# Optimization experiments

Measured on AMD Instinct MI355X. Metric: run time of the kernel, lower is better.

The kernel has to match this reference:

```python
import jax, jax.numpy as jnp
import numpy as np

B, T = 64, 512
OBS, DM, DS, NL = 115, 128, 8, 3
EMB, NA, H1 = 16, 19, 256


def _ln(x, g, b, eps=1e-5):
    m = jnp.mean(x, -1, keepdims=True)
    v = jnp.mean((x - m) ** 2, -1, keepdims=True)
    return (x - m) * jax.lax.rsqrt(v + eps) * g + b


def _s6(x, h, lng, lnb, w_ig, w_dt, b_dt, a_log, w_b, w_c, d_par, w_out):
    # x: [B,T,DM], h: [B,DM,DS]
    xn = _ln(x, lng, lnb)
    xp = xn @ w_ig.T                               # [B,T,2*DM]
    x_in, z = xp[..., :DM], xp[..., DM:]
    dt = jax.nn.softplus(x_in @ w_dt.T + b_dt)     # [B,T,DM]
    A = -jnp.exp(a_log)                            # [DM,DS]
    bt = x_in @ w_b.T                              # [B,T,DS]
    ct = x_in @ w_c.T                              # [B,T,DS]
    dA = jnp.exp(dt[..., None] * A)                # [B,T,DM,DS]
    upd = (dt * x_in)[..., None] * bt[:, :, None, :]  # [B,T,DM,DS]

    def step(hc, inp):
        dA_t, u_t, c_t = inp
        hn = dA_t * hc + u_t                       # [B,DM,DS]
        y = jnp.einsum('bds,bs->bd', hn, c_t)      # [B,DM]
        return hn, y

    h_f, ys = jax.lax.scan(
        step, h,
        (jnp.swapaxes(dA, 0, 1), jnp.swapaxes(upd, 0, 1), jnp.swapaxes(ct, 0, 1)))
    y = jnp.swapaxes(ys, 0, 1)                     # [B,T,DM]
    ssm = y * jax.nn.silu(z) + x_in * d_par
    return x + ssm @ w_out.T, h_f.reshape(h_f.shape[0], -1)


def _forward(prev_actions, obs, h0, enc_w1, enc_b1, enc_g1, enc_bb1, enc_w2, enc_b2,
             enc_g2, enc_bb2, emb, proj_w, proj_b, proj_g, proj_bb,
             m_ln_g, m_ln_b, m_w_ig, m_w_dt, m_b_dt, m_a_log, m_w_b, m_w_c, m_d, m_w_out,
             fn_g, fn_b, pol_w1, pol_b1, pol_g, pol_bb, pol_w2, pol_b2):
    # MLP encoder: Linear -> LN -> SiLU -> Linear -> LN (final norm)
    e = jax.nn.silu(_ln(obs @ enc_w1.T + enc_b1, enc_g1, enc_bb1))
    e = _ln(e @ enc_w2.T + enc_b2, enc_g2, enc_bb2)
    pa = emb[prev_actions]                         # [B,T,EMB]
    x = jnp.concatenate([e, pa], -1) @ proj_w.T + proj_b
    x = jax.nn.silu(_ln(x, proj_g, proj_bb))
    for i in range(NL):
        x, _ = _s6(x, h0[i].reshape(-1, DM, DS), m_ln_g[i], m_ln_b[i], m_w_ig[i],
                   m_w_dt[i], m_b_dt[i], m_a_log[i], m_w_b[i], m_w_c[i], m_d[i], m_w_out[i])
    x = _ln(x, fn_g, fn_b)
    p = jax.nn.silu(_ln(x @ pol_w1.T + pol_b1, pol_g, pol_bb))
    return p @ pol_w2.T + pol_b2                   # [B,T,NA] policy logits


def setup_inputs() -> dict:
    key = jax.random.key(0)
    ks = iter(jax.random.split(key, 64))
    def n(shape, s=0.05):
        return jax.random.normal(next(ks), shape, dtype=jnp.float32) * s
    return {
        'obs': jax.random.normal(next(ks), (B, T, OBS), dtype=jnp.float32),
        'h0': jnp.zeros((NL, B, DM * DS), jnp.float32),
        'enc_w1': n((H1, OBS)), 'enc_b1': jnp.zeros((H1,)),
        'enc_g1': jnp.ones((H1,)), 'enc_bb1': jnp.zeros((H1,)),
        'enc_w2': n((DM, H1)), 'enc_b2': jnp.zeros((DM,)),
        'enc_g2': jnp.ones((DM,)), 'enc_bb2': jnp.zeros((DM,)),
        'emb': n((NA + 1, EMB), 1.0),
        'proj_w': n((DM, DM + EMB)), 'proj_b': jnp.zeros((DM,)),
        'proj_g': jnp.ones((DM,)), 'proj_bb': jnp.zeros((DM,)),
        'm_ln_g': jnp.ones((NL, DM)), 'm_ln_b': jnp.zeros((NL, DM)),
        'm_w_ig': n((NL, 2 * DM, DM)), 'm_w_dt': n((NL, DM, DM)),
        'm_b_dt': jnp.zeros((NL, DM)),
        'm_a_log': jax.random.uniform(next(ks), (NL, DM, DS), minval=-3.0, maxval=-1.0, dtype=jnp.float32),
        'm_w_b': n((NL, DS, DM)), 'm_w_c': n((NL, DS, DM)),
        'm_d': jnp.ones((NL, DM)), 'm_w_out': n((NL, DM, DM)),
        'fn_g': jnp.ones((DM,)), 'fn_b': jnp.zeros((DM,)),
        'pol_w1': n((DM, DM)), 'pol_b1': jnp.zeros((DM,)),
        'pol_g': jnp.ones((DM,)), 'pol_bb': jnp.zeros((DM,)),
        'pol_w2': n((NA, DM)), 'pol_b2': jnp.zeros((NA,)),
        'prev_actions': jax.random.randint(next(ks), (B, T), 0, NA + 1),
    }


def reference(obs, h0, enc_w1, enc_b1, enc_g1, enc_bb1, enc_w2, enc_b2, enc_g2, enc_bb2,
              emb, proj_w, proj_b, proj_g, proj_bb, m_ln_g, m_ln_b, m_w_ig, m_w_dt,
              m_b_dt, m_a_log, m_w_b, m_w_c, m_d, m_w_out, fn_g, fn_b, pol_w1, pol_b1,
              pol_g, pol_bb, pol_w2, pol_b2, prev_actions):
    return _forward(prev_actions, obs, h0, enc_w1, enc_b1, enc_g1, enc_bb1, enc_w2,
                    enc_b2, enc_g2, enc_bb2, emb, proj_w, proj_b, proj_g, proj_bb,
                    m_ln_g, m_ln_b, m_w_ig, m_w_dt, m_b_dt, m_a_log, m_w_b, m_w_c,
                    m_d, m_w_out, fn_g, fn_b, pol_w1, pol_b1, pol_g, pol_bb, pol_w2, pol_b2)
```

## Files before the change

### kernel.cpp

```cpp
#include <hip/hip_runtime.h>
#include <math.h>

#define BB 64
#define TT 512
#define OBSD 115
#define DMD 128
#define DSD 8
#define NLD 3
#define EMBD 16
#define NAD 19
#define H1D 256
#define NTOK (BB*TT)
#define SSEG 16
#define TSEG (TT/SSEG)

typedef unsigned short ushort_t;
typedef __attribute__((ext_vector_type(8))) short short8;
typedef __attribute__((ext_vector_type(4))) float f32x4;

__device__ __forceinline__ float silu_f(float x){ return x / (1.f + __expf(-x)); }
__device__ __forceinline__ float softplus_f(float x){
  return fmaxf(x, 0.f) + log1pf(__expf(-fabsf(x)));
}
__device__ __forceinline__ ushort_t f2bf(float x){
  unsigned u = __float_as_uint(x);
  unsigned r = (u + 0x7fffu + ((u >> 16) & 1u)) >> 16;
  return (ushort_t)r;
}
__device__ __forceinline__ float b2f(ushort_t x){
  return __uint_as_float(((unsigned)x) << 16);
}
#define MFMA(a,b,c) __builtin_amdgcn_mfma_f32_16x16x32_bf16((a),(b),(c),0,0,0)
#define LOG2E 1.44269504f

template<int D, int SV>
__device__ __forceinline__ void ln32(const float* s_val, float* s_mr, int tid){
  const int t = tid >> 3, part = tid & 7;
  float s = 0.f, s2 = 0.f;
  #pragma unroll
  for (int j = part; j < D; j += 8){ float v = s_val[t*SV + j]; s += v; s2 = fmaf(v, v, s2); }
  s += __shfl_xor(s, 1, 64); s2 += __shfl_xor(s2, 1, 64);
  s += __shfl_xor(s, 2, 64); s2 += __shfl_xor(s2, 2, 64);
  s += __shfl_xor(s, 4, 64); s2 += __shfl_xor(s2, 4, 64);
  if (part == 0){
    float m = s * (1.f/(float)D);
    s_mr[t*2] = m;
    s_mr[t*2+1] = rsqrtf(s2 * (1.f/(float)D) - m*m + 1e-5f);
  }
}

struct PJob { const float* src; ushort_t* dst; int N; int K; int Kpad; int rowofs; int Nw; };
struct PJobs { PJob j[20]; };

__global__ __launch_bounds__(256) void k_prep(PJobs P){
  const int job = blockIdx.x >> 2;
  const int sub = blockIdx.x & 3;
  PJob pj = P.j[job];
  const int elems = pj.Nw * pj.Kpad;
  for (int idx = sub*256 + threadIdx.x; idx < elems; idx += 4*256){
    int n = idx / pj.Kpad;
    int k = idx - n*pj.Kpad;
    float v = (n < pj.N && k < pj.K) ? pj.src[(size_t)n*pj.K + k] : 0.f;
    pj.dst[(size_t)(pj.rowofs + n)*pj.Kpad + k] = f2bf(v);
  }
}

__global__ __launch_bounds__(256) void k_enc1(
    const float* __restrict__ obs, const ushort_t* __restrict__ w1b,
    const float* __restrict__ b1, const float* __restrict__ g1,
    const float* __restrict__ bb1, ushort_t* __restrict__ e1)
{
  __shared__ __align__(16) char sm[34048];
  float*    s_val = (float*)sm;
  ushort_t* s_a   = (ushort_t*)sm;
  float*    s_mr  = (float*)(sm + 33792);
  const int tok0 = blockIdx.x * 32;
  const int tid = threadIdx.x;
  const int lane = tid & 63, w = tid >> 6;
  const int q = lane >> 4, cn = lane & 15;
  const int m0 = (w & 1) * 16, nh = w >> 1;

  for (int e = tid; e < 32*16; e += 256){
    int t = e >> 4, kc = e & 15;
    const float* op = obs + (size_t)(tok0 + t)*OBSD;
    short8 v;
    #pragma unroll
    for (int j = 0; j < 8; j++){
      int k = kc*8 + j;
      v[j] = (short)f2bf(k < OBSD ? op[k] : 0.f);
    }
    *(short8*)&s_a[t*136 + kc*8] = v;
  }
  __syncthreads();

  short8 af[4];
  #pragma unroll
  for (int ks = 0; ks < 4; ks++)
    af[ks] = *(const short8*)&s_a[(m0 + cn)*136 + ks*32 + q*8];
  __syncthreads();

  #pragma unroll
  for (int nt = 0; nt < 8; nt++){
    const int n0 = (nh*8 + nt) * 16;
    f32x4 acc = {0.f,0.f,0.f,0.f};
    #pragma unroll
    for (int ks = 0; ks < 4; ks++){
      short8 bf = *(const short8*)&w1b[(size_t)(n0 + cn)*128 + ks*32 + q*8];
      acc = MFMA(af[ks], bf, acc);
    }
    float bias = b1[n0 + cn];
    #pragma unroll
    for (int r = 0; r < 4; r++)
      s_val[(m0 + q*4 + r)*264 + n0 + cn] = acc[r] + bias;
  }
  __syncthreads();

  ln32<256,264>(s_val, s_mr, tid);
  __syncthreads();
  for (int e = tid; e < 32*256; e += 256){
    int t = e >> 8, c = e & 255;
    float v = (s_val[t*264 + c] - s_mr[t*2]) * s_mr[t*2+1] * g1[c] + bb1[c];
    e1[(size_t)(tok0 + t)*256 + c] = f2bf(silu_f(v));
  }
}

__global__ __launch_bounds__(256) void k_enc2p(
    const ushort_t* __restrict__ e1, const ushort_t* __restrict__ w2b,
    const float* __restrict__ b2, const float* __restrict__ g2,
    const float* __restrict__ bb2,
    const float* __restrict__ emb, const int* __restrict__ pact,
    const ushort_t* __restrict__ pwb, const float* __restrict__ pb,
    const float* __restrict__ pg, const float* __restrict__ pbb,
    float* __restrict__ X,
    const float* __restrict__ lng, const float* __restrict__ lnb,
    const ushort_t* __restrict__ wigb, const ushort_t* __restrict__ wdbcb,
    const float* __restrict__ bdt,
    ushort_t* __restrict__ XINb, ushort_t* __restrict__ Zb,
    ushort_t* __restrict__ DTb, ushort_t* __restrict__ BTu, ushort_t* __restrict__ CTu,
    const float* __restrict__ alog0,
    float* __restrict__ HLOC, float* __restrict__ PPR)
{
  __shared__ __align__(16) char sm[28928];
  float*    s_val = (float*)sm;
  ushort_t* s_xin = (ushort_t*)sm;
  ushort_t* s_dt  = (ushort_t*)(sm + 8704);
  ushort_t* s_a   = (ushort_t*)(sm + 17408);
  ushort_t* s_btc = (ushort_t*)(sm + 28160);
  float*    s_mr  = (float*)(sm + 28672);

  const int tok0 = blockIdx.x * 32;
  const int bidx = blockIdx.x >> 4;
  const int ch   = blockIdx.x & 15;
  const int tid = threadIdx.x;
  const int lane = tid & 63, w = tid >> 6;
  const int q = lane >> 4, cn = lane & 15;
  const int m0 = (w & 1) * 16, nh = w >> 1;

  for (int e = tid; e < 32*32; e += 256){
    int t = e >> 5, k = e & 31;
    float v = 0.f;
    if (k < EMBD){ int a = pact[tok0 + t]; v = emb[(size_t)a*EMBD + k]; }
    s_a[t*168 + 128 + k] = f2bf(v);
  }
  {
    short8 af[8];
    #pragma unroll
    for (int ks = 0; ks < 8; ks++)
      af[ks] = *(const short8*)&e1[(size_t)(tok0 + m0 + cn)*256 + ks*32 + q*8];
    #pragma unroll
    for (int nt = 0; nt < 4; nt++){
      const int n0 = (nh*4 + nt) * 16;
      f32x4 acc = {0.f,0.f,0.f,0.f};
      #pragma unroll
      for (int ks = 0; ks < 8; ks++){
        short8 bf = *(const short8*)&w2b[(size_t)(n0 + cn)*256 + ks*32 + q*8];
        acc = MFMA(af[ks], bf, acc);
      }
      float bias = b2[n0 + cn];
      #pragma unroll
      for (int r = 0; r < 4; r++)
        s_val[(m0 + q*4 + r)*136 + n0 + cn] = acc[r] + bias;
    }
  }
  __syncthreads();

  ln32<128,136>(s_val, s_mr, tid);
  __syncthreads();
  for (int e = tid; e < 32*128; e += 256){
    int t = e >> 7, c = e & 127;
    float v = (s_val[t*136 + c] - s_mr[t*2]) * s_mr[t*2+1] * g2[c] + bb2[c];
    s_a[t*168 + c] = f2bf(v);
  }
  __syncthreads();

  {
    short8 af2[5];
    #pragma unroll
    for (int ks = 0; ks < 5; ks++)
      af2[ks] = *(const short8*)&s_a[(m0 + cn)*168 + ks*32 + q*8];
    #pragma unroll
    for (int nt = 0; nt < 4; nt++){
      const int n0 = (nh*4 + nt) * 16;
      f32x4 acc = {0.f,0.f,0.f,0.f};
      #pragma unroll
      for (int ks = 0; ks < 5; ks++){
        short8 bf = *(const short8*)&pwb[(size_t)(n0 + cn)*160 + ks*32 + q*8];
        acc = MFMA(af2[ks], bf, acc);
      }
      float bias = pb[n0 + cn];
      #pragma unroll
      for (int r = 0; r < 4; r++)
        s_val[(m0 + q*4 + r)*136 + n0 + cn] = acc[r] + bias;
    }
  }
  __syncthreads();

  ln32<128,136>(s_val, s_mr, tid);
  __syncthreads();
  for (int e = tid; e < 32*128; e += 256){
    int t = e >> 7, c = e & 127;
    float v = (s_val[t*136 + c] - s_mr[t*2]) * s_mr[t*2+1] * pg[c] + pbb[c];
    v = silu_f(v);
    X[(size_t)tok0*128 + e] = v;
    s_val[t*136 + c] = v;
  }
  __syncthreads();

  ln32<128,136>(s_val, s_mr, tid);
  __syncthreads();
  for (int e = tid; e < 32*128; e += 256){
    int t = e >> 7, c = e & 127;
    float v = (s_val[t*136 + c] - s_mr[t*2]) * s_mr[t*2+1] * lng[c] + lnb[c];
    s_a[t*168 + c] = f2bf(v);
  }
  __syncthreads();

  {
    short8 af[4];
    #pragma unroll
    for (int ks = 0; ks < 4; ks++)
      af[ks] = *(const short8*)&s_a[(m0 + cn)*168 + ks*32 + q*8];
    #pragma unroll
    for (int nt = 0; nt < 8; nt++){
      const int n0 = (nh*8 + nt) * 16;
      f32x4 acc = {0.f,0.f,0.f,0.f};
      #pragma unroll
      for (int ks = 0; ks < 4; ks++){
        short8 bf = *(const short8*)&wigb[(size_t)(n0 + cn)*128 + ks*32 + q*8];
        acc = MFMA(af[ks], bf, acc);
      }
      if (n0 < 128){
        #pragma unroll
        for (int r = 0; r < 4; r++){
          int tr = m0 + q*4 + r;
          ushort_t bb = f2bf(acc[r]);
          XINb[(size_t)(tok0 + tr)*128 + n0 + cn] = bb;
          s_xin[tr*136 + n0 + cn] = bb;
        }
      } else {
        #pragma unroll
        for (int r = 0; r < 4; r++){
          int tr = m0 + q*4 + r;
          Zb[(size_t)(tok0 + tr)*128 + (n0 - 128) + cn] = f2bf(acc[r]);
        }
      }
    }
  }
  __syncthreads();

  {
    short8 af2[4];
    #pragma unroll
    for (int ks = 0; ks < 4; ks++)
      af2[ks] = *(const short8*)&s_xin[(m0 + cn)*136 + ks*32 + q*8];
    for (int nt = nh; nt < 9; nt += 2){
      const int n0 = nt * 16;
      f32x4 acc = {0.f,0.f,0.f,0.f};
      #pragma unroll
      for (int ks = 0; ks < 4; ks++){
        short8 bf = *(const short8*)&wdbcb[(size_t)(n0 + cn)*128 + ks*32 + q*8];
        acc = MFMA(af2[ks], bf, acc);
      }
      const int col = n0 + cn;
      if (col < 128){
        float bd = bdt[col];
        #pragma unroll
        for (int r = 0; r < 4; r++){
          int tr = m0 + q*4 + r;
          ushort_t dv = f2bf(softplus_f(acc[r] + bd));
          DTb[(size_t)(tok0 + tr)*128 + col] = dv;
          s_dt[tr*136 + col] = dv;
        }
      } else if (col < 136){
        #pragma unroll
        for (int r = 0; r < 4; r++){
          int tr = m0 + q*4 + r;
          ushort_t bb = f2bf(acc[r]);
          BTu[(size_t)(tok0 + tr)*8 + (col - 128)] = bb;
          s_btc[tr*8 + (col - 128)] = bb;
        }
      } else {
        #pragma unroll
        for (int r = 0; r < 4; r++)
          CTu[(size_t)(tok0 + m0 + q*4 + r)*8 + (col - 136)] = f2bf(acc[r]);
      }
    }
  }
  __syncthreads();

  {
    const int d = tid & 127, sh = tid >> 7;
    float A2c[4], hh[4], pp[4];
    #pragma unroll
    for (int j = 0; j < 4; j++){
      A2c[j] = -__expf(alog0[d*8 + sh*4 + j]) * LOG2E;
      hh[j] = 0.f; pp[j] = 1.f;
    }
    for (int t = 0; t < 32; t++){
      float dt = b2f(s_dt[t*136 + d]);
      float wv = dt * b2f(s_xin[t*136 + d]);
      #pragma unroll
      for (int j = 0; j < 4; j++){
        float dA = exp2f(dt * A2c[j]);
        hh[j] = fmaf(dA, hh[j], wv * b2f(s_btc[t*8 + sh*4 + j]));
        pp[j] *= dA;
      }
    }
    const size_t o = ((size_t)bidx*16 + ch)*1024 + d*8 + sh*4;
    #pragma unroll
    for (int j = 0; j < 4; j++){ HLOC[o+j] = hh[j]; PPR[o+j] = pp[j]; }
  }
}

#define SMS 26368

__device__ __forceinline__ void phaseB_post(
    const ushort_t* DTb, const ushort_t* XINb, const ushort_t* Zb,
    const ushort_t* BTu, const ushort_t* CTu,
    const float* __restrict__ alog, const float* __restrict__ h0g,
    const float* __restrict__ HLi, const float* __restrict__ PPi,
    const float* __restrict__ dpar, const ushort_t* __restrict__ woutb,
    float* __restrict__ X, char* sm, int b, int sg, int tid)
{
  ushort_t* s_dtS = (ushort_t*)sm;
  ushort_t* s_xiS = (ushort_t*)(sm + 8192);
  ushort_t* s_a   = (ushort_t*)(sm + 16384);
  float*    s_x   = (float*)sm;
  ushort_t* s_bt  = (ushort_t*)(sm + 25088);
  ushort_t* s_ct  = (ushort_t*)(sm + 25600);
  float*    s_mr  = (float*)(sm + 26112);

  const int d = tid;
  const int w = tid >> 6, lane = tid & 63, q = lane >> 4, cn = lane & 15;
  const size_t segtok = (size_t)b*TT + sg*TSEG;

  {
    const uint4* gdt = (const uint4*)(DTb + segtok*128);
    const uint4* gxi = (const uint4*)(XINb + segtok*128);
    #pragma unroll
    for (int i = 0; i < 4; i++){
      ((uint4*)s_dtS)[tid + i*128] = gdt[tid + i*128];
      ((uint4*)s_xiS)[tid + i*128] = gxi[tid + i*128];
    }
    ((unsigned*)s_bt)[tid] = ((const unsigned*)(BTu + segtok*8))[tid];
    ((unsigned*)s_ct)[tid] = ((const unsigned*)(CTu + segtok*8))[tid];
  }
  float A2[8], h[8];
  #pragma unroll
  for (int s = 0; s < 8; s++){
    A2[s] = -__expf(alog[d*8 + s]) * LOG2E;
    h[s] = h0g[(size_t)b*1024 + d*8 + s];
  }
  for (int ch = 0; ch < sg; ch++){
    const size_t o = ((size_t)b*SSEG + ch)*1024 + d*8;
    float4 hl0 = *(const float4*)(HLi + o);
    float4 hl1 = *(const float4*)(HLi + o + 4);
    float4 pp0 = *(const float4*)(PPi + o);
    float4 pp1 = *(const float4*)(PPi + o + 4);
    h[0]=fmaf(pp0.x,h[0],hl0.x); h[1]=fmaf(pp0.y,h[1],hl0.y);
    h[2]=fmaf(pp0.z,h[2],hl0.z); h[3]=fmaf(pp0.w,h[3],hl0.w);
    h[4]=fmaf(pp1.x,h[4],hl1.x); h[5]=fmaf(pp1.y,h[5],hl1.y);
    h[6]=fmaf(pp1.z,h[6],hl1.z); h[7]=fmaf(pp1.w,h[7],hl1.w);
  }
  __syncthreads();

  #pragma unroll 4
  for (int t = 0; t < 32; t++){
    float dt = b2f(s_dtS[t*128 + d]);
    float xi = b2f(s_xiS[t*128 + d]);
    float wv = dt * xi;
    float y = 0.f;
    #pragma unroll
    for (int s = 0; s < 8; s++){
      float dA = exp2f(dt * A2[s]);
      h[s] = fmaf(dA, h[s], wv * b2f(s_bt[t*8 + s]));
      y = fmaf(h[s], b2f(s_ct[t*8 + s]), y);
    }
    s_a[t*136 + d] = f2bf(y);
  }
  __syncthreads();

  {
    const int c0 = (tid & 15)*8, trow = tid >> 4;
    float dpv[8];
    #pragma unroll
    for (int j = 0; j < 8; j++) dpv[j] = dpar[c0 + j];
    #pragma unroll
    for (int i = 0; i < 4; i++){
      const int t = trow + i*8;
      uint4 zb = ((const uint4*)(Zb + segtok*128))[tid + i*128];
      const ushort_t* zp = (const ushort_t*)&zb;
      #pragma unroll
      for (int j = 0; j < 8; j++){
        float y  = b2f(s_a[t*136 + c0 + j]);
        float xi = b2f(s_xiS[t*128 + c0 + j]);
        float ssm = y * silu_f(b2f(zp[j])) + xi * dpv[j];
        s_a[t*136 + c0 + j] = f2bf(ssm);
      }
    }
  }
  __syncthreads();

  {
    short8 af[2][4];
    #pragma unroll
    for (int mt = 0; mt < 2; mt++)
      #pragma unroll
      for (int ks = 0; ks < 4; ks++)
        af[mt][ks] = *(const short8*)&s_a[(mt*16 + cn)*136 + ks*32 + q*8];
    __syncthreads();
    for (int nt = w; nt < 8; nt += 2){
      const int n0 = nt * 16;
      short8 bf[4];
      #pragma unroll
      for (int ks = 0; ks < 4; ks++)
        bf[ks] = *(const short8*)&woutb[(size_t)(n0+cn)*128 + ks*32 + q*8];
      #pragma unroll
      for (int mt = 0; mt < 2; mt++){
        f32x4 acc = {0.f,0.f,0.f,0.f};
        #pragma unroll
        for (int ks = 0; ks < 4; ks++) acc = MFMA(af[mt][ks], bf[ks], acc);
        #pragma unroll
        for (int r = 0; r < 4; r++){
          const int tr = mt*16 + q*4 + r;
          const size_t g = (segtok + tr)*128 + n0 + cn;
          float xn = X[g] + acc[r];
          X[g] = xn;
          s_x[tr*130 + n0 + cn] = xn;
        }
      }
    }
  }
  __syncthreads();

  {
    const int t = tid >> 2, qtr = tid & 3;
    float s = 0.f, s2 = 0.f;
    const float* row = s_x + t*130 + qtr*32;
    for (int j = 0; j < 32; j++){ float v = row[j]; s += v; s2 = fmaf(v, v, s2); }
    s  += __shfl_xor(s, 1, 64);  s2 += __shfl_xor(s2, 1, 64);
    s  += __shfl_xor(s, 2, 64);  s2 += __shfl_xor(s2, 2, 64);
    float m = s * (1.f/128.f);
    float var = s2 * (1.f/128.f) - m*m;
    if (qtr == 0){ s_mr[t*2] = m; s_mr[t*2+1] = rsqrtf(var + 1e-5f); }
  }
  __syncthreads();
}

__global__ __launch_bounds__(256) void k_scan2p(
    ushort_t* DTb, ushort_t* XINb, ushort_t* Zb,
    ushort_t* BTu, ushort_t* CTu,
    const float* __restrict__ alog, const float* __restrict__ h0g,
    const float* __restrict__ HLi, const float* __restrict__ PPi,
    const float* __restrict__ dpar, const ushort_t* __restrict__ woutb,
    float* __restrict__ X,
    const float* __restrict__ lng, const float* __restrict__ lnb,
    const ushort_t* __restrict__ wigb, const ushort_t* __restrict__ wdbcb,
    const float* __restrict__ bdt,
    const float* __restrict__ alogn,
    float* __restrict__ HLo, float* __restrict__ PPo)
{
  __shared__ __align__(16) char sm_all[2*SMS];
  const int sub = threadIdx.x >> 7;
  char* sm = sm_all + sub*SMS;
  const int tid = threadIdx.x & 127;

  ushort_t* s_a  = (ushort_t*)(sm + 16384);
  float*    s_x  = (float*)sm;
  ushort_t* s_xin= (ushort_t*)sm;
  ushort_t* s_bt = (ushort_t*)(sm + 25088);
  float*    s_mr = (float*)(sm + 26112);

  const int b = blockIdx.x >> 3;
  const int sg = (blockIdx.x & 7)*2 + sub;
  const int w = tid >> 6, lane = tid & 63, q = lane >> 4, cn = lane & 15;
  const size_t segtok = (size_t)b*TT + sg*TSEG;

  phaseB_post(DTb, XINb, Zb, BTu, CTu, alog, h0g, HLi, PPi, dpar, woutb, X, sm, b, sg, tid);

  {
    float g = lng[tid], c0 = lnb[tid];
    float x31 = s_x[31*130 + tid];
    __syncthreads();
    for (int t = 0; t < 31; t++){
      float v = (s_x[t*130 + tid] - s_mr[t*2]) * s_mr[t*2+1] * g + c0;
      s_a[t*136 + tid] = f2bf(v);
    }
    float v = (x31 - s_mr[62]) * s_mr[63] * g + c0;
    s_a[31*136 + tid] = f2bf(v);
  }
  __syncthreads();

  {
    short8 af[2][4];
    #pragma unroll
    for (int mt = 0; mt < 2; mt++)
      #pragma unroll
      for (int ks = 0; ks < 4; ks++)
        af[mt][ks] = *(const short8*)&s_a[(mt*16 + cn)*136 + ks*32 + q*8];
    for (int nt = w; nt < 16; nt += 2){
      const int n0 = nt * 16;
      short8 bf[4];
      #pragma unroll
      for (int ks = 0; ks < 4; ks++)
        bf[ks] = *(const short8*)&wigb[(size_t)(n0+cn)*128 + ks*32 + q*8];
      #pragma unroll
      for (int mt = 0; mt < 2; mt++){
        f32x4 acc = {0.f,0.f,0.f,0.f};
        #pragma unroll
        for (int ks = 0; ks < 4; ks++) acc = MFMA(af[mt][ks], bf[ks], acc);
        if (n0 < 128){
          #pragma unroll
          for (int r = 0; r < 4; r++){
            const int tr = mt*16 + q*4 + r;
            ushort_t bb = f2bf(acc[r]);
            XINb[(segtok + tr)*128 + n0 + cn] = bb;
            s_xin[tr*136 + n0 + cn] = bb;
          }
        } else {
          #pragma unroll
          for (int r = 0; r < 4; r++){
            const int tr = mt*16 + q*4 + r;
            Zb[(segtok + tr)*128 + (n0-128) + cn] = f2bf(acc[r]);
          }
        }
      }
    }
  }
  __syncthreads();

  {
    short8 af[2][4];
    #pragma unroll
    for (int mt = 0; mt < 2; mt++)
      #pragma unroll
      for (int ks = 0; ks < 4; ks++)
        af[mt][ks] = *(const short8*)&s_xin[(mt*16 + cn)*136 + ks*32 + q*8];
    for (int nt = w; nt < 9; nt += 2){
      const int n0 = nt * 16;
      short8 bf[4];
      #pragma unroll
      for (int ks = 0; ks < 4; ks++)
        bf[ks] = *(const short8*)&wdbcb[(size_t)(n0+cn)*128 + ks*32 + q*8];
      const int col = n0 + cn;
      #pragma unroll
      for (int mt = 0; mt < 2; mt++){
        f32x4 acc = {0.f,0.f,0.f,0.f};
        #pragma unroll
        for (int ks = 0; ks < 4; ks++) acc = MFMA(af[mt][ks], bf[ks], acc);
        if (col < 128){
          float bd = bdt[col];
          #pragma unroll
          for (int r = 0; r < 4; r++){
            const int tr = mt*16 + q*4 + r;
            ushort_t dv = f2bf(softplus_f(acc[r] + bd));
            DTb[(segtok + tr)*128 + col] = dv;
            s_a[tr*136 + col] = dv;
          }
        } else if (col < 136){
          #pragma unroll
          for (int r = 0; r < 4; r++){
            const int tr = mt*16 + q*4 + r;
            ushort_t bb = f2bf(acc[r]);
            BTu[(segtok + tr)*8 + (col-128)] = bb;
            s_bt[tr*8 + (col-128)] = bb;
          }
        } else {
          #pragma unroll
          for (int r = 0; r < 4; r++)
            CTu[(segtok + mt*16 + q*4 + r)*8 + (col-136)] = f2bf(acc[r]);
        }
      }
    }
  }
  __syncthreads();

  {
    float A2n[8], hh[8], pp[8];
    #pragma unroll
    for (int s = 0; s < 8; s++){
      A2n[s] = -__expf(alogn[tid*8 + s]) * LOG2E;
      hh[s] = 0.f; pp[s] = 1.f;
    }
    for (int t = 0; t < 32; t++){
      float dt = b2f(s_a[t*136 + tid]);
      float wv = dt * b2f(s_xin[t*136 + tid]);
      #pragma unroll
      for (int s = 0; s < 8; s++){
        float dA = exp2f(dt * A2n[s]);
        hh[s] = fmaf(dA, hh[s], wv * b2f(s_bt[t*8 + s]));
        pp[s] *= dA;
      }
    }
    const size_t o = ((size_t)b*SSEG + sg)*1024 + tid*8;
    #pragma unroll
    for (int s = 0; s < 8; s++){ HLo[o+s] = hh[s]; PPo[o+s] = pp[s]; }
  }
}

__global__ __launch_bounds__(256) void k_scan2h(
    const ushort_t* DTb, const ushort_t* XINb, const ushort_t* Zb,
    const ushort_t* BTu, const ushort_t* CTu,
    const float* __restrict__ alog, const float* __restrict__ h0g,
    const float* __restrict__ HLi, const float* __restrict__ PPi,
    const float* __restrict__ dpar, const ushort_t* __restrict__ woutb,
    float* __restrict__ X,
    const float* __restrict__ fng, const float* __restrict__ fnb,
    const ushort_t* __restrict__ pw1b, const float* __restrict__ pb1,
    const float* __restrict__ pg, const float* __restrict__ pbb,
    const ushort_t* __restrict__ pw2b, const float* __restrict__ pb2,
    float* __restrict__ out)
{
  __shared__ __align__(16) char sm_all[2*SMS];
  const int sub = threadIdx.x >> 7;
  char* sm = sm_all + sub*SMS;
  const int tid = threadIdx.x & 127;

  ushort_t* s_a  = (ushort_t*)(sm + 16384);
  float*    s_x  = (float*)sm;
  float*    s_mr = (float*)(sm + 26112);

  const int b = blockIdx.x >> 3;
  const int sg = (blockIdx.x & 7)*2 + sub;
  const int w = tid >> 6, lane = tid & 63, q = lane >> 4, cn = lane & 15;
  const size_t segtok = (size_t)b*TT + sg*TSEG;

  phaseB_post((ushort_t*)DTb, (ushort_t*)XINb, (ushort_t*)Zb,
              (ushort_t*)BTu, (ushort_t*)CTu, alog, h0g, HLi, PPi,
              dpar, woutb, X, sm, b, sg, tid);

  {
    float g = fng[tid], c0 = fnb[tid];
    float x31 = s_x[31*130 + tid];
    __syncthreads();
    for (int t = 0; t < 31; t++){
      float v = (s_x[t*130 + tid] - s_mr[t*2]) * s_mr[t*2+1] * g + c0;
      s_a[t*136 + tid] = f2bf(v);
    }
    float v = (x31 - s_mr[62]) * s_mr[63] * g + c0;
    s_a[31*136 + tid] = f2bf(v);
  }
  __syncthreads();

  {
    short8 af[2][4];
    #pragma unroll
    for (int mt = 0; mt < 2; mt++)
      #pragma unroll
      for (int ks = 0; ks < 4; ks++)
        af[mt][ks] = *(const short8*)&s_a[(mt*16 + cn)*136 + ks*32 + q*8];
    __syncthreads();
    for (int nt = w; nt < 8; nt += 2){
      const int n0 = nt * 16;
      short8 bf[4];
      #pragma unroll
      for (int ks = 0; ks < 4; ks++)
        bf[ks] = *(const short8*)&pw1b[(size_t)(n0+cn)*128 + ks*32 + q*8];
      float bias = pb1[n0 + cn];
      #pragma unroll
      for (int mt = 0; mt < 2; mt++){
        f32x4 acc = {0.f,0.f,0.f,0.f};
        #pragma unroll
        for (int ks = 0; ks < 4; ks++) acc = MFMA(af[mt][ks], bf[ks], acc);
        #pragma unroll
        for (int r = 0; r < 4; r++)
          s_x[(mt*16 + q*4 + r)*130 + n0 + cn] = acc[r] + bias;
      }
    }
  }
  __syncthreads();

  {
    const int t = tid >> 2, qtr = tid & 3;
    float s = 0.f, s2 = 0.f;
    const float* row = s_x + t*130 + qtr*32;
    for (int j = 0; j < 32; j++){ float v = row[j]; s += v; s2 = fmaf(v, v, s2); }
    s  += __shfl_xor(s, 1, 64);  s2 += __shfl_xor(s2, 1, 64);
    s  += __shfl_xor(s, 2, 64);  s2 += __shfl_xor(s2, 2, 64);
    float m = s * (1.f/128.f);
    float var = s2 * (1.f/128.f) - m*m;
    if (qtr == 0){ s_mr[t*2] = m; s_mr[t*2+1] = rsqrtf(var + 1e-5f); }
  }
  __syncthreads();
  {
    float g = pg[tid], c0 = pbb[tid];
    float x31 = s_x[31*130 + tid];
    __syncthreads();
    for (int t = 0; t < 31; t++){
      float v = (s_x[t*130 + tid] - s_mr[t*2]) * s_mr[t*2+1] * g + c0;
      s_a[t*136 + tid] = f2bf(silu_f(v));
    }
    float v = (x31 - s_mr[62]) * s_mr[63] * g + c0;
    s_a[31*136 + tid] = f2bf(silu_f(v));
  }
  __syncthreads();

  {
    short8 af[2][4];
    #pragma unroll
    for (int mt = 0; mt < 2; mt++)
      #pragma unroll
      for (int ks = 0; ks < 4; ks++)
        af[mt][ks] = *(const short8*)&s_a[(mt*16 + cn)*136 + ks*32 + q*8];
    const int n0 = w * 16;
    short8 bf[4];
    #pragma unroll
    for (int ks = 0; ks < 4; ks++)
      bf[ks] = *(const short8*)&pw2b[(size_t)(n0+cn)*128 + ks*32 + q*8];
    const int col = n0 + cn;
    #pragma unroll
    for (int mt = 0; mt < 2; mt++){
      f32x4 acc = {0.f,0.f,0.f,0.f};
      #pragma unroll
      for (int ks = 0; ks < 4; ks++) acc = MFMA(af[mt][ks], bf[ks], acc);
      if (col < NAD){
        float bias = pb2[col];
        #pragma unroll
        for (int r = 0; r < 4; r++)
          out[(segtok + mt*16 + q*4 + r)*NAD + col] = acc[r] + bias;
      }
    }
  }
}

extern "C" void kernel_launch(void* const* d_in, const int* in_sizes, int n_in,
                              void* d_out, int out_size, void* d_ws, size_t ws_size,
                              hipStream_t stream) {
  const float* obs    = (const float*)d_in[0];
  const float* h0     = (const float*)d_in[1];
  const float* enc_w1 = (const float*)d_in[2];
  const float* enc_b1 = (const float*)d_in[3];
  const float* enc_g1 = (const float*)d_in[4];
  const float* enc_bb1= (const float*)d_in[5];
  const float* enc_w2 = (const float*)d_in[6];
  const float* enc_b2 = (const float*)d_in[7];
  const float* enc_g2 = (const float*)d_in[8];
  const float* enc_bb2= (const float*)d_in[9];
  const float* emb    = (const float*)d_in[10];
  const float* proj_w = (const float*)d_in[11];
  const float* proj_b = (const float*)d_in[12];
  const float* proj_g = (const float*)d_in[13];
  const float* proj_bb= (const float*)d_in[14];
  const float* m_ln_g = (const float*)d_in[15];
  const float* m_ln_b = (const float*)d_in[16];
  const float* m_w_ig = (const float*)d_in[17];
  const float* m_w_dt = (const float*)d_in[18];
  const float* m_b_dt = (const float*)d_in[19];
  const float* m_a_log= (const float*)d_in[20];
  const float* m_w_b  = (const float*)d_in[21];
  const float* m_w_c  = (const float*)d_in[22];
  const float* m_d    = (const float*)d_in[23];
  const float* m_w_out= (const float*)d_in[24];
  const float* fn_g   = (const float*)d_in[25];
  const float* fn_b   = (const float*)d_in[26];
  const float* pol_w1 = (const float*)d_in[27];
  const float* pol_b1 = (const float*)d_in[28];
  const float* pol_g  = (const float*)d_in[29];
  const float* pol_bb = (const float*)d_in[30];
  const float* pol_w2 = (const float*)d_in[31];
  const float* pol_b2 = (const float*)d_in[32];
  const int*   pact   = (const int*)d_in[33];

  float* ws  = (float*)d_ws;
  float* X    = ws;
  float* HLA  = X + (size_t)NTOK*128;
  float* PPA  = HLA + (size_t)BB*SSEG*1024;
  float* HLB  = PPA + (size_t)BB*SSEG*1024;
  float* PPB  = HLB + (size_t)BB*SSEG*1024;
  ushort_t* E1   = (ushort_t*)(PPB + (size_t)BB*SSEG*1024);
  ushort_t* XINb = E1   + (size_t)NTOK*256;
  ushort_t* Zb   = XINb + (size_t)NTOK*128;
  ushort_t* DTb  = Zb   + (size_t)NTOK*128;
  ushort_t* BTu  = DTb  + (size_t)NTOK*128;
  ushort_t* CTu  = BTu  + (size_t)NTOK*8;

  ushort_t* W1B   = CTu   + (size_t)NTOK*8;
  ushort_t* W2B   = W1B   + 256*128;
  ushort_t* PWB   = W2B   + 128*256;
  ushort_t* WIGB  = PWB   + 128*160;
  ushort_t* WDBCB = WIGB  + 3*256*128;
  ushort_t* WOUTB = WDBCB + 3*144*128;
  ushort_t* PW1B  = WOUTB + 3*128*128;
  ushort_t* PW2B  = PW1B  + 128*128;

  PJobs P;
  int nj = 0;
  auto add = [&](const float* src, ushort_t* dst, int N, int K, int Kpad, int rowofs, int Nw){
    P.j[nj].src = src; P.j[nj].dst = dst; P.j[nj].N = N; P.j[nj].K = K;
    P.j[nj].Kpad = Kpad; P.j[nj].rowofs = rowofs; P.j[nj].Nw = Nw; nj++;
  };
  add(enc_w1, W1B, 256, 115, 128, 0, 256);
  add(enc_w2, W2B, 128, 256, 256, 0, 128);
  add(proj_w, PWB, 128, 144, 160, 0, 128);
  for (int l = 0; l < NLD; l++)
    add(m_w_ig + (size_t)l*256*128, WIGB + (size_t)l*256*128, 256, 128, 128, 0, 256);
  for (int l = 0; l < NLD; l++){
    add(m_w_dt + (size_t)l*128*128, WDBCB + (size_t)l*144*128, 128, 128, 128, 0,   128);
    add(m_w_b  + (size_t)l*8*128,   WDBCB + (size_t)l*144*128,   8, 128, 128, 128,   8);
    add(m_w_c  + (size_t)l*8*128,   WDBCB + (size_t)l*144*128,   8, 128, 128, 136,   8);
  }
  for (int l = 0; l < NLD; l++)
    add(m_w_out + (size_t)l*128*128, WOUTB + (size_t)l*128*128, 128, 128, 128, 0, 128);
  add(pol_w1, PW1B, 128, 128, 128, 0, 128);
  add(pol_w2, PW2B,  19, 128, 128, 0,  32);

  k_prep<<<20*4, 256, 0, stream>>>(P);
  k_enc1<<<NTOK/32, 256, 0, stream>>>(obs, W1B, enc_b1, enc_g1, enc_bb1, E1);
  k_enc2p<<<NTOK/32, 256, 0, stream>>>(E1, W2B, enc_b2, enc_g2, enc_bb2,
      emb, pact, PWB, proj_b, proj_g, proj_bb, X,
      m_ln_g, m_ln_b, WIGB, WDBCB, m_b_dt,
      XINb, Zb, DTb, BTu, CTu,
      m_a_log, HLA, PPA);

  const int scangrid = BB*SSEG/2;
  k_scan2p<<<scangrid, 256, 0, stream>>>(DTb, XINb, Zb, BTu, CTu,
      m_a_log, h0, HLA, PPA, m_d, WOUTB, X,
      m_ln_g + 128, m_ln_b + 128,
      WIGB + (size_t)256*128, WDBCB + (size_t)144*128, m_b_dt + 128,
      m_a_log + 1024, HLB, PPB);
  k_scan2p<<<scangrid, 256, 0, stream>>>(DTb, XINb, Zb, BTu, CTu,
      m_a_log + 1024, h0 + (size_t)BB*1024, HLB, PPB, m_d + 128,
      WOUTB + (size_t)128*128, X,
      m_ln_g + 256, m_ln_b + 256,
      WIGB + (size_t)2*256*128, WDBCB + (size_t)2*144*128, m_b_dt + 256,
      m_a_log + 2048, HLA, PPA);
  k_scan2h<<<scangrid, 256, 0, stream>>>(DTb, XINb, Zb, BTu, CTu,
      m_a_log + 2048, h0 + (size_t)2*BB*1024, HLA, PPA, m_d + 256,
      WOUTB + (size_t)2*128*128, X,
      fn_g, fn_b, PW1B, pol_b1, pol_g, pol_bb, PW2B, pol_b2,
      (float*)d_out);
}
```

Before: 401.7 us.

## Double scan segment count to halve per-block sequence length and shared memory

Splits each sequence into 32 segments of 16 tokens instead of 16 of 32. The per-segment GEMMs shrink to a single 16-row MFMA tile, the shared-memory footprint per sub-block halves, and the chunk-summary pass splits each 32-token chunk into two 16-token halves. The aim is to double the number of independent blocks and shorten the serial recurrence per thread, so the GPU is better occupied. In exchange the cross-segment prefix combine loop gets longer, each block does less MFMA work per weight load, and the HLB/PPB state buffers now alias the E1 workspace region.

After: 466.8 us. 1.16x slower.

```diff
diff --git a/kernel.cpp b/kernel.cpp
--- a/kernel.cpp
+++ b/kernel.cpp
@@ -11,7 +11,7 @@
 #define NAD 19
 #define H1D 256
 #define NTOK (BB*TT)
-#define SSEG 16
+#define SSEG 32
 #define TSEG (TT/SSEG)
 
 typedef unsigned short ushort_t;
@@ -309,30 +309,33 @@
   __syncthreads();
 
   {
-    const int d = tid & 127, sh = tid >> 7;
-    float A2c[4], hh[4], pp[4];
-    #pragma unroll
-    for (int j = 0; j < 4; j++){
-      A2c[j] = -__expf(alog0[d*8 + sh*4 + j]) * LOG2E;
-      hh[j] = 0.f; pp[j] = 1.f;
-    }
-    for (int t = 0; t < 32; t++){
+    const int d = tid & 127, half = tid >> 7;
+    float A2c[8], hh[8], pp[8];
+    #pragma unroll
+    for (int s = 0; s < 8; s++){
+      A2c[s] = -__expf(alog0[d*8 + s]) * LOG2E;
+      hh[s] = 0.f; pp[s] = 1.f;
+    }
+    const int t0 = half * 16;
+    #pragma unroll 4
+    for (int tt = 0; tt < 16; tt++){
+      const int t = t0 + tt;
       float dt = b2f(s_dt[t*136 + d]);
       float wv = dt * b2f(s_xin[t*136 + d]);
       #pragma unroll
-      for (int j = 0; j < 4; j++){
-        float dA = exp2f(dt * A2c[j]);
-        hh[j] = fmaf(dA, hh[j], wv * b2f(s_btc[t*8 + sh*4 + j]));
-        pp[j] *= dA;
-      }
-    }
-    const size_t o = ((size_t)bidx*16 + ch)*1024 + d*8 + sh*4;
-    #pragma unroll
-    for (int j = 0; j < 4; j++){ HLOC[o+j] = hh[j]; PPR[o+j] = pp[j]; }
-  }
-}
-
-#define SMS 26368
+      for (int s = 0; s < 8; s++){
+        float dA = exp2f(dt * A2c[s]);
+        hh[s] = fmaf(dA, hh[s], wv * b2f(s_btc[t*8 + s]));
+        pp[s] *= dA;
+      }
+    }
+    const size_t o = ((size_t)bidx*SSEG + ch*2 + half)*1024 + d*8;
+    #pragma unroll
+    for (int s = 0; s < 8; s++){ HLOC[o+s] = hh[s]; PPR[o+s] = pp[s]; }
+  }
+}
+
+#define SMS 13440
 
 __device__ __forceinline__ void phaseB_post(
     const ushort_t* DTb, const ushort_t* XINb, const ushort_t* Zb,
@@ -343,12 +346,12 @@
     float* __restrict__ X, char* sm, int b, int sg, int tid)
 {
   ushort_t* s_dtS = (ushort_t*)sm;
-  ushort_t* s_xiS = (ushort_t*)(sm + 8192);
-  ushort_t* s_a   = (ushort_t*)(sm + 16384);
+  ushort_t* s_xiS = (ushort_t*)(sm + 4096);
   float*    s_x   = (float*)sm;
-  ushort_t* s_bt  = (ushort_t*)(sm + 25088);
-  ushort_t* s_ct  = (ushort_t*)(sm + 25600);
-  float*    s_mr  = (float*)(sm + 26112);
+  ushort_t* s_a   = (ushort_t*)(sm + 8320);
+  ushort_t* s_bt  = (ushort_t*)(sm + 12672);
+  ushort_t* s_ct  = (ushort_t*)(sm + 12928);
+  float*    s_mr  = (float*)(sm + 13184);
 
   const int d = tid;
   const int w = tid >> 6, lane = tid & 63, q = lane >> 4, cn = lane & 15;
@@ -358,12 +361,14 @@
     const uint4* gdt = (const uint4*)(DTb + segtok*128);
     const uint4* gxi = (const uint4*)(XINb + segtok*128);
     #pragma unroll
-    for (int i = 0; i < 4; i++){
+    for (int i = 0; i < 2; i++){
       ((uint4*)s_dtS)[tid + i*128] = gdt[tid + i*128];
       ((uint4*)s_xiS)[tid + i*128] = gxi[tid + i*128];
     }
-    ((unsigned*)s_bt)[tid] = ((const unsigned*)(BTu + segtok*8))[tid];
-    ((unsigned*)s_ct)[tid] = ((const unsigned*)(CTu + segtok*8))[tid];
+    if (tid < 64){
+      ((unsigned*)s_bt)[tid] = ((const unsigned*)(BTu + segtok*8))[tid];
+      ((unsigned*)s_ct)[tid] = ((const unsigned*)(CTu + segtok*8))[tid];
+    }
   }
   float A2[8], h[8];
   #pragma unroll
@@ -385,7 +390,7 @@
   __syncthreads();
 
   #pragma unroll 4
-  for (int t = 0; t < 32; t++){
+  for (int t = 0; t < TSEG; t++){
     float dt = b2f(s_dtS[t*128 + d]);
     float xi = b2f(s_xiS[t*128 + d]);
     float wv = dt * xi;
@@ -406,7 +411,7 @@
     #pragma unroll
     for (int j = 0; j < 8; j++) dpv[j] = dpar[c0 + j];
     #pragma unroll
-    for (int i = 0; i < 4; i++){
+    for (int i = 0; i < 2; i++){
       const int t = trow + i*8;
       uint4 zb = ((const uint4*)(Zb + segtok*128))[tid + i*128];
       const ushort_t* zp = (const ushort_t*)&zb;
@@ -422,47 +427,45 @@
   __syncthreads();
 
   {
-    short8 af[2][4];
-    #pragma unroll
-    for (int mt = 0; mt < 2; mt++)
-      #pragma unroll
-      for (int ks = 0; ks < 4; ks++)
-        af[mt][ks] = *(const short8*)&s_a[(mt*16 + cn)*136 + ks*32 + q*8];
-    __syncthreads();
+    short8 af[4];
+    #pragma unroll
+    for (int ks = 0; ks < 4; ks++)
+      af[ks] = *(const short8*)&s_a[cn*136 + ks*32 + q*8];
     for (int nt = w; nt < 8; nt += 2){
       const int n0 = nt * 16;
       short8 bf[4];
       #pragma unroll
       for (int ks = 0; ks < 4; ks++)
         bf[ks] = *(const short8*)&woutb[(size_t)(n0+cn)*128 + ks*32 + q*8];
-      #pragma unroll
-      for (int mt = 0; mt < 2; mt++){
-        f32x4 acc = {0.f,0.f,0.f,0.f};
-        #pragma unroll
-        for (int ks = 0; ks < 4; ks++) acc = MFMA(af[mt][ks], bf[ks], acc);
-        #pragma unroll
-        for (int r = 0; r < 4; r++){
-          const int tr = mt*16 + q*4 + r;
-          const size_t g = (segtok + tr)*128 + n0 + cn;
-          float xn = X[g] + acc[r];
-          X[g] = xn;
-          s_x[tr*130 + n0 + cn] = xn;
-        }
-      }
-    }
-  }
-  __syncthreads();
-
-  {
-    const int t = tid >> 2, qtr = tid & 3;
+      f32x4 acc = {0.f,0.f,0.f,0.f};
+      #pragma unroll
+      for (int ks = 0; ks < 4; ks++) acc = MFMA(af[ks], bf[ks], acc);
+      #pragma unroll
+      for (int r = 0; r < 4; r++){
+        const int tr = q*4 + r;
+        const size_t g = (segtok + tr)*128 + n0 + cn;
+        float xn = X[g] + acc[r];
+        X[g] = xn;
+        s_x[tr*130 + n0 + cn] = xn;
+      }
+    }
+  }
+  __syncthreads();
+
+  {
+    const int t = tid >> 3, part = tid & 7;
     float s = 0.f, s2 = 0.f;
-    const float* row = s_x + t*130 + qtr*32;
-    for (int j = 0; j < 32; j++){ float v = row[j]; s += v; s2 = fmaf(v, v, s2); }
+    const float* row = s_x + t*130 + part*16;
+    #pragma unroll
+    for (int j = 0; j < 16; j++){ float v = row[j]; s += v; s2 = fmaf(v, v, s2); }
     s  += __shfl_xor(s, 1, 64);  s2 += __shfl_xor(s2, 1, 64);
     s  += __shfl_xor(s, 2, 64);  s2 += __shfl_xor(s2, 2, 64);
-    float m = s * (1.f/128.f);
-    float var = s2 * (1.f/128.f) - m*m;
-    if (qtr == 0){ s_mr[t*2] = m; s_mr[t*2+1] = rsqrtf(var + 1e-5f); }
+    s  += __shfl_xor(s, 4, 64);  s2 += __shfl_xor(s2, 4, 64);
+    if (part == 0){
+      float m = s * (1.f/128.f);
+      s_mr[t*2] = m;
+      s_mr[t*2+1] = rsqrtf(s2 * (1.f/128.f) - m*m + 1e-5f);
+    }
   }
   __syncthreads();
 }
@@ -485,77 +488,67 @@
   char* sm = sm_all + sub*SMS;
   const int tid = threadIdx.x & 127;
 
-  ushort_t* s_a  = (ushort_t*)(sm + 16384);
   float*    s_x  = (float*)sm;
   ushort_t* s_xin= (ushort_t*)sm;
-  ushort_t* s_bt = (ushort_t*)(sm + 25088);
-  float*    s_mr = (float*)(sm + 26112);
-
-  const int b = blockIdx.x >> 3;
-  const int sg = (blockIdx.x & 7)*2 + sub;
+  ushort_t* s_a  = (ushort_t*)(sm + 8320);
+  ushort_t* s_bt = (ushort_t*)(sm + 12672);
+  float*    s_mr = (float*)(sm + 13184);
+
+  const int b = blockIdx.x >> 4;
+  const int sg = (blockIdx.x & 15)*2 + sub;
   const int w = tid >> 6, lane = tid & 63, q = lane >> 4, cn = lane & 15;
   const size_t segtok = (size_t)b*TT + sg*TSEG;
 
   phaseB_post(DTb, XINb, Zb, BTu, CTu, alog, h0g, HLi, PPi, dpar, woutb, X, sm, b, sg, tid);
 
   {
-    float g = lng[tid], c0 = lnb[tid];
-    float x31 = s_x[31*130 + tid];
-    __syncthreads();
-    for (int t = 0; t < 31; t++){
-      float v = (s_x[t*130 + tid] - s_mr[t*2]) * s_mr[t*2+1] * g + c0;
+    float g = lng[tid], c0v = lnb[tid];
+    #pragma unroll
+    for (int t = 0; t < TSEG; t++){
+      float v = (s_x[t*130 + tid] - s_mr[t*2]) * s_mr[t*2+1] * g + c0v;
       s_a[t*136 + tid] = f2bf(v);
     }
-    float v = (x31 - s_mr[62]) * s_mr[63] * g + c0;
-    s_a[31*136 + tid] = f2bf(v);
-  }
-  __syncthreads();
-
-  {
-    short8 af[2][4];
-    #pragma unroll
-    for (int mt = 0; mt < 2; mt++)
-      #pragma unroll
-      for (int ks = 0; ks < 4; ks++)
-        af[mt][ks] = *(const short8*)&s_a[(mt*16 + cn)*136 + ks*32 + q*8];
+  }
+  __syncthreads();
+
+  {
+    short8 af[4];
+    #pragma unroll
+    for (int ks = 0; ks < 4; ks++)
+      af[ks] = *(const short8*)&s_a[cn*136 + ks*32 + q*8];
     for (int nt = w; nt < 16; nt += 2){
       const int n0 = nt * 16;
       short8 bf[4];
       #pragma unroll
       for (int ks = 0; ks < 4; ks++)
         bf[ks] = *(const short8*)&wigb[(size_t)(n0+cn)*128 + ks*32 + q*8];
-      #pragma unroll
-      for (int mt = 0; mt < 2; mt++){
-        f32x4 acc = {0.f,0.f,0.f,0.f};
-        #pragma unroll
-        for (int ks = 0; ks < 4; ks++) acc = MFMA(af[mt][ks], bf[ks], acc);
-        if (n0 < 128){
-          #pragma unroll
-          for (int r = 0; r < 4; r++){
-            const int tr = mt*16 + q*4 + r;
-            ushort_t bb = f2bf(acc[r]);
-            XINb[(segtok + tr)*128 + n0 + cn] = bb;
-            s_xin[tr*136 + n0 + cn] = bb;
-          }
-        } else {
-          #pragma unroll
-          for (int r = 0; r < 4; r++){
-            const int tr = mt*16 + q*4 + r;
-            Zb[(segtok + tr)*128 + (n0-128) + cn] = f2bf(acc[r]);
-          }
+      f32x4 acc = {0.f,0.f,0.f,0.f};
+      #pragma unroll
+      for (int ks = 0; ks < 4; ks++) acc = MFMA(af[ks], bf[ks], acc);
+      if (n0 < 128){
+        #pragma unroll
+        for (int r = 0; r < 4; r++){
+          const int tr = q*4 + r;
+          ushort_t bb = f2bf(acc[r]);
+          XINb[(segtok + tr)*128 + n0 + cn] = bb;
+          s_xin[tr*136 + n0 + cn] = bb;
         }
-      }
-    }
-  }
-  __syncthreads();
-
-  {
-    short8 af[2][4];
-    #pragma unroll
-    for (int mt = 0; mt < 2; mt++)
-      #pragma unroll
-      for (int ks = 0; ks < 4; ks++)
-        af[mt][ks] = *(const short8*)&s_xin[(mt*16 + cn)*136 + ks*32 + q*8];
+      } else {
+        #pragma unroll
+        for (int r = 0; r < 4; r++){
+          const int tr = q*4 + r;
+          Zb[(segtok + tr)*128 + (n0-128) + cn] = f2bf(acc[r]);
+        }
+      }
+    }
+  }
+  __syncthreads();
+
+  {
+    short8 af2[4];
+    #pragma unroll
+    for (int ks = 0; ks < 4; ks++)
+      af2[ks] = *(const short8*)&s_xin[cn*136 + ks*32 + q*8];
     for (int nt = w; nt < 9; nt += 2){
       const int n0 = nt * 16;
       short8 bf[4];
@@ -563,33 +556,30 @@
       for (int ks = 0; ks < 4; ks++)
         bf[ks] = *(const short8*)&wdbcb[(size_t)(n0+cn)*128 + ks*32 + q*8];
       const int col = n0 + cn;
-      #pragma unroll
-      for (int mt = 0; mt < 2; mt++){
-        f32x4 acc = {0.f,0.f,0.f,0.f};
-        #pragma unroll
-        for (int ks = 0; ks < 4; ks++) acc = MFMA(af[mt][ks], bf[ks], acc);
-        if (col < 128){
-          float bd = bdt[col];
-          #pragma unroll
-          for (int r = 0; r < 4; r++){
-            const int tr = mt*16 + q*4 + r;
-            ushort_t dv = f2bf(softplus_f(acc[r] + bd));
-            DTb[(segtok + tr)*128 + col] = dv;
-            s_a[tr*136 + col] = dv;
-          }
-        } else if (col < 136){
-          #pragma unroll
-          for (int r = 0; r < 4; r++){
-            const int tr = mt*16 + q*4 + r;
-            ushort_t bb = f2bf(acc[r]);
-            BTu[(segtok + tr)*8 + (col-128)] = bb;
-            s_bt[tr*8 + (col-128)] = bb;
-          }
-        } else {
-          #pragma unroll
-          for (int r = 0; r < 4; r++)
-            CTu[(segtok + mt*16 + q*4 + r)*8 + (col-136)] = f2bf(acc[r]);
+      f32x4 acc = {0.f,0.f,0.f,0.f};
+      #pragma unroll
+      for (int ks = 0; ks < 4; ks++) acc = MFMA(af2[ks], bf[ks], acc);
+      if (col < 128){
+        float bd = bdt[col];
+        #pragma unroll
+        for (int r = 0; r < 4; r++){
+          const int tr = q*4 + r;
+          ushort_t dv = f2bf(softplus_f(acc[r] + bd));
+          DTb[(segtok + tr)*128 + col] = dv;
+          s_a[tr*136 + col] = dv;
         }
+      } else if (col < 136){
+        #pragma unroll
+        for (int r = 0; r < 4; r++){
+          const int tr = q*4 + r;
+          ushort_t bb = f2bf(acc[r]);
+          BTu[(segtok + tr)*8 + (col-128)] = bb;
+          s_bt[tr*8 + (col-128)] = bb;
+        }
+      } else {
+        #pragma unroll
+        for (int r = 0; r < 4; r++)
+          CTu[(segtok + q*4 + r)*8 + (col-136)] = f2bf(acc[r]);
       }
     }
   }
@@ -602,7 +592,8 @@
       A2n[s] = -__expf(alogn[tid*8 + s]) * LOG2E;
       hh[s] = 0.f; pp[s] = 1.f;
     }
-    for (int t = 0; t < 32; t++){
+    #pragma unroll 4
+    for (int t = 0; t < TSEG; t++){
       float dt = b2f(s_a[t*136 + tid]);
       float wv = dt * b2f(s_xin[t*136 + tid]);
       #pragma unroll
@@ -636,12 +627,12 @@
   char* sm = sm_all + sub*SMS;
   const int tid = threadIdx.x & 127;
 
-  ushort_t* s_a  = (ushort_t*)(sm + 16384);
   float*    s_x  = (float*)sm;
-  float*    s_mr = (float*)(sm + 26112);
-
-  const int b = blockIdx.x >> 3;
-  const int sg = (blockIdx.x & 7)*2 + sub;
+  ushort_t* s_a  = (ushort_t*)(sm + 8320);
+  float*    s_mr = (float*)(sm + 13184);
+
+  const int b = blockIdx.x >> 4;
+  const int sg = (blockIdx.x & 15)*2 + sub;
   const int w = tid >> 6, lane = tid & 63, q = lane >> 4, cn = lane & 15;
   const size_t segtok = (size_t)b*TT + sg*TSEG;
 
@@ -650,26 +641,20 @@
               dpar, woutb, X, sm, b, sg, tid);
 
   {
-    float g = fng[tid], c0 = fnb[tid];
-    float x31 = s_x[31*130 + tid];
-    __syncthreads();
-    for (int t = 0; t < 31; t++){
-      float v = (s_x[t*130 + tid] - s_mr[t*2]) * s_mr[t*2+1] * g + c0;
+    float g = fng[tid], c0v = fnb[tid];
+    #pragma unroll
+    for (int t = 0; t < TSEG; t++){
+      float v = (s_x[t*130 + tid] - s_mr[t*2]) * s_mr[t*2+1] * g + c0v;
       s_a[t*136 + tid] = f2bf(v);
     }
-    float v = (x31 - s_mr[62]) * s_mr[63] * g + c0;
-    s_a[31*136 + tid] = f2bf(v);
-  }
-  __syncthreads();
-
-  {
-    short8 af[2][4];
-    #pragma unroll
-    for (int mt = 0; mt < 2; mt++)
-      #pragma unroll
-      for (int ks = 0; ks < 4; ks++)
-        af[mt][ks] = *(const short8*)&s_a[(mt*16 + cn)*136 + ks*32 + q*8];
-    __syncthreads();
+  }
+  __syncthreads();
+
+  {
+    short8 af[4];
+    #pragma unroll
+    for (int ks = 0; ks < 4; ks++)
+      af[ks] = *(const short8*)&s_a[cn*136 + ks*32 + q*8];
     for (int nt = w; nt < 8; nt += 2){
       const int n0 = nt * 16;
       short8 bf[4];
@@ -677,68 +662,61 @@
       for (int ks = 0; ks < 4; ks++)
         bf[ks] = *(const short8*)&pw1b[(size_t)(n0+cn)*128 + ks*32 + q*8];
       float bias = pb1[n0 + cn];
-      #pragma unroll
-      for (int mt = 0; mt < 2; mt++){
-        f32x4 acc = {0.f,0.f,0.f,0.f};
-        #pragma unroll
-        for (int ks = 0; ks < 4; ks++) acc = MFMA(af[mt][ks], bf[ks], acc);
-        #pragma unroll
-        for (int r = 0; r < 4; r++)
-          s_x[(mt*16 + q*4 + r)*130 + n0 + cn] = acc[r] + bias;
-      }
-    }
-  }
-  __syncthreads();
-
-  {
-    const int t = tid >> 2, qtr = tid & 3;
+      f32x4 acc = {0.f,0.f,0.f,0.f};
+      #pragma unroll
+      for (int ks = 0; ks < 4; ks++) acc = MFMA(af[ks], bf[ks], acc);
+      #pragma unroll
+      for (int r = 0; r < 4; r++)
+        s_x[(q*4 + r)*130 + n0 + cn] = acc[r] + bias;
+    }
+  }
+  __syncthreads();
+
+  {
+    const int t = tid >> 3, part = tid & 7;
     float s = 0.f, s2 = 0.f;
-    const float* row = s_x + t*130 + qtr*32;
-    for (int j = 0; j < 32; j++){ float v = row[j]; s += v; s2 = fmaf(v, v, s2); }
+    const float* row = s_x + t*130 + part*16;
+    #pragma unroll
+    for (int j = 0; j < 16; j++){ float v = row[j]; s += v; s2 = fmaf(v, v, s2); }
     s  += __shfl_xor(s, 1, 64);  s2 += __shfl_xor(s2, 1, 64);
     s  += __shfl_xor(s, 2, 64);  s2 += __shfl_xor(s2, 2, 64);
-    float m = s * (1.f/128.f);
-    float var = s2 * (1.f/128.f) - m*m;
-    if (qtr == 0){ s_mr[t*2] = m; s_mr[t*2+1] = rsqrtf(var + 1e-5f); }
-  }
-  __syncthreads();
-  {
-    float g = pg[tid], c0 = pbb[tid];
-    float x31 = s_x[31*130 + tid];
-    __syncthreads();
-    for (int t = 0; t < 31; t++){
-      float v = (s_x[t*130 + tid] - s_mr[t*2]) * s_mr[t*2+1] * g + c0;
+    s  += __shfl_xor(s, 4, 64);  s2 += __shfl_xor(s2, 4, 64);
+    if (part == 0){
+      float m = s * (1.f/128.f);
+      s_mr[t*2] = m;
+      s_mr[t*2+1] = rsqrtf(s2 * (1.f/128.f) - m*m + 1e-5f);
+    }
+  }
+  __syncthreads();
+  {
+    float g = pg[tid], c0v = pbb[tid];
+    #pragma unroll
+    for (int t = 0; t < TSEG; t++){
+      float v = (s_x[t*130 + tid] - s_mr[t*2]) * s_mr[t*2+1] * g + c0v;
       s_a[t*136 + tid] = f2bf(silu_f(v));
     }
-    float v = (x31 - s_mr[62]) * s_mr[63] * g + c0;
-    s_a[31*136 + tid] = f2bf(silu_f(v));
-  }
-  __syncthreads();
-
-  {
-    short8 af[2][4];
-    #pragma unroll
-    for (int mt = 0; mt < 2; mt++)
-      #pragma unroll
-      for (int ks = 0; ks < 4; ks++)
-        af[mt][ks] = *(const short8*)&s_a[(mt*16 + cn)*136 + ks*32 + q*8];
+  }
+  __syncthreads();
+
+  {
+    short8 af[4];
+    #pragma unroll
+    for (int ks = 0; ks < 4; ks++)
+      af[ks] = *(const short8*)&s_a[cn*136 + ks*32 + q*8];
     const int n0 = w * 16;
     short8 bf[4];
     #pragma unroll
     for (int ks = 0; ks < 4; ks++)
       bf[ks] = *(const short8*)&pw2b[(size_t)(n0+cn)*128 + ks*32 + q*8];
     const int col = n0 + cn;
-    #pragma unroll
-    for (int mt = 0; mt < 2; mt++){
-      f32x4 acc = {0.f,0.f,0.f,0.f};
-      #pragma unroll
-      for (int ks = 0; ks < 4; ks++) acc = MFMA(af[mt][ks], bf[ks], acc);
-      if (col < NAD){
-        float bias = pb2[col];
-        #pragma unroll
-        for (int r = 0; r < 4; r++)
-          out[(segtok + mt*16 + q*4 + r)*NAD + col] = acc[r] + bias;
-      }
+    f32x4 acc = {0.f,0.f,0.f,0.f};
+    #pragma unroll
+    for (int ks = 0; ks < 4; ks++) acc = MFMA(af[ks], bf[ks], acc);
+    if (col < NAD){
+      float bias = pb2[col];
+      #pragma unroll
+      for (int r = 0; r < 4; r++)
+        out[(segtok + q*4 + r)*NAD + col] = acc[r] + bias;
     }
   }
 }
@@ -785,9 +763,9 @@
   float* X    = ws;
   float* HLA  = X + (size_t)NTOK*128;
   float* PPA  = HLA + (size_t)BB*SSEG*1024;
-  float* HLB  = PPA + (size_t)BB*SSEG*1024;
+  ushort_t* E1 = (ushort_t*)(PPA + (size_t)BB*SSEG*1024);
+  float* HLB  = (float*)E1;
   float* PPB  = HLB + (size_t)BB*SSEG*1024;
-  ushort_t* E1   = (ushort_t*)(PPB + (size_t)BB*SSEG*1024);
   ushort_t* XINb = E1   + (size_t)NTOK*256;
   ushort_t* Zb   = XINb + (size_t)NTOK*128;
   ushort_t* DTb  = Zb   + (size_t)NTOK*128;
```
